# Kernel optimization log

Hardware: AMD Instinct MI355X
Metric: run time of the kernel (lower is better)

The kernel has to match this reference:

```python
import jax, jax.numpy as jnp
import numpy as np

# Assumptions from DCalhas/eeg_to_fmri repo layers:
#  - RandomFourierFeatures: z = cos(x @ W + b) followed by layer normalization
#    over the feature axis (normalization='layer'), W/b trainable.
#  - Sinusoids: elementwise sin(x).

B, D, T, L = 64, 512, 1024, 512

def _layer_norm(x, eps=1e-5):
    mu = jnp.mean(x, axis=-1, keepdims=True)
    var = jnp.var(x, axis=-1, keepdims=True)
    return (x - mu) * jax.lax.rsqrt(var + eps)

def setup_inputs() -> dict:
    key = jax.random.key(0)
    ks = jax.random.split(key, 12)
    s = 1.0 / np.sqrt(L)
    return {
        "x": jax.random.normal(ks[0], (B, D, T), jnp.float32),
        "rff_w": jax.random.normal(ks[1], (D, L), jnp.float32) * (1.0 / np.sqrt(D)),
        "rff_b": jax.random.uniform(ks[2], (L,), jnp.float32, 0.0, 2.0 * np.pi),
        "weight_input": jax.random.normal(ks[3], (L, L), jnp.float32) * s,
        "weight_forget": jax.random.normal(ks[4], (L, L), jnp.float32) * s,
        "weight_context": jax.random.normal(ks[5], (L, L), jnp.float32) * s,
        "recurrent_input": jax.random.normal(ks[6], (L, L), jnp.float32) * s,
        "recurrent_forget": jax.random.normal(ks[7], (L, L), jnp.float32) * s,
        "recurrent_context": jax.random.normal(ks[8], (L, L), jnp.float32) * s,
        "bias_input": jnp.zeros((L,), jnp.float32),
        "bias_forget": jnp.zeros((L,), jnp.float32),
        "bias_context": jnp.zeros((L,), jnp.float32),
        "init_latent": jax.random.normal(ks[9], (1, 1, L), jnp.float32) * s,
        "init_context": jax.random.normal(ks[10], (1, 1, L), jnp.float32) * s,
    }

def reference(x, rff_w, rff_b, weight_input, weight_forget, weight_context,
              recurrent_input, recurrent_forget, recurrent_context,
              bias_input, bias_forget, bias_context, init_latent, init_context):
    b = x.shape[0]
    xt = jnp.transpose(x, (0, 2, 1))                      # [B,T,D]
    z = _layer_norm(jnp.cos(xt @ rff_w + rff_b))          # [B,T,L]
    # hidden_states[t+1] = z_t in the original loop, so the "recurrent" input
    # at step t is z_{t-1} (init_latent at t=0). Gates are thus batchable.
    z_prev = jnp.concatenate(
        [jnp.broadcast_to(init_latent, (b, 1, z.shape[2])), z[:, :-1]], axis=1)
    i = jax.nn.sigmoid(z @ weight_input + z_prev @ recurrent_input + bias_input)
    f = jax.nn.sigmoid(z @ weight_forget + z_prev @ recurrent_forget + bias_forget)
    g = jnp.tanh(z @ weight_context + z_prev @ recurrent_context + bias_context)
    o = jnp.sin(z)                                        # Sinusoids gate

    c0 = jnp.broadcast_to(init_context[:, 0], (b, z.shape[2]))  # [B,L]
    def step(c_prev, gates):
        i_t, f_t, g_t, o_t = gates
        c_t = f_t * c_prev + i_t * g_t
        return c_t, o_t * c_t
    xs = tuple(jnp.transpose(a, (1, 0, 2)) for a in (i, f, g, o))  # time-major
    _, h = jax.lax.scan(step, c0, xs)                     # [T,B,L]
    return jnp.transpose(h, (1, 2, 0))                    # [B,L,T]
```

## Files before the change

### kernel.cpp

```cpp
#include <hip/hip_runtime.h>
#include <hip/hip_bf16.h>
#include <hip/hip_fp16.h>
#include <cstdint>
#include <cstddef>


typedef float f32x4 __attribute__((ext_vector_type(4)));
typedef short s16x8 __attribute__((ext_vector_type(8)));

__device__ __forceinline__ void gload_lds16(const void* g, void* l) {
  __builtin_amdgcn_global_load_lds(
      (const __attribute__((address_space(1))) void*)g,
      (__attribute__((address_space(3))) void*)l, 16, 0, 0);
}
__device__ __forceinline__ ushort f2bf(float f) {
  uint32_t u = __float_as_uint(f);
  return (ushort)((u + 0x7FFF + ((u >> 16) & 1)) >> 16);
}
__device__ __forceinline__ float bf2f(ushort s) {
  return __uint_as_float(((uint32_t)s) << 16);
}
__device__ __forceinline__ ushort f2h(float f) {
  return __half_as_ushort(__float2half(f));
}
__device__ __forceinline__ float h2f(ushort s) {
  return __half2float(__ushort_as_half(s));
}

#define MF(d, a, b) d = __builtin_amdgcn_mfma_f32_16x16x32_bf16(a, b, d, 0, 0, 0);

__global__ __launch_bounds__(256) void prep_all(
    const float* __restrict__ s0, const float* __restrict__ s1,
    const float* __restrict__ s2, const float* __restrict__ s3,
    const float* __restrict__ s4, const float* __restrict__ s5,
    const float* __restrict__ il, const float* __restrict__ W1,
    const float* __restrict__ x,
    ushort* __restrict__ W2t, ushort* __restrict__ ilb,
    ushort* __restrict__ W1t, ushort* __restrict__ xt)
{
  __shared__ float tile[64][68];
  const int z = blockIdx.z;
  if (z >= 8) {
    if (blockIdx.y >= 8) return;
    const int b = z - 8;
    const int t0 = blockIdx.x * 64, d0 = blockIdx.y * 64;
    const float* src = x + ((size_t)b * 512 + d0) * 1024 + t0;
    const int lr_ = threadIdx.x >> 4, lc4 = (threadIdx.x & 15) * 4;
#pragma unroll
    for (int p = 0; p < 4; ++p) {
      const float4 v = *(const float4*)(src + (size_t)(lr_ + p * 16) * 1024 + lc4);
      *(float4*)&tile[lr_ + p * 16][lc4] = v;
    }
    __syncthreads();
    const int tt = threadIdx.x >> 2, dc = (threadIdx.x & 3) * 16;
    ushort* dst = xt + ((size_t)b * 1024 + t0 + tt) * 512 + d0 + dc;
    uint4 o1, o2;
    o1.x = (uint)f2bf(tile[dc + 0][tt]) | ((uint)f2bf(tile[dc + 1][tt]) << 16);
    o1.y = (uint)f2bf(tile[dc + 2][tt]) | ((uint)f2bf(tile[dc + 3][tt]) << 16);
    o1.z = (uint)f2bf(tile[dc + 4][tt]) | ((uint)f2bf(tile[dc + 5][tt]) << 16);
    o1.w = (uint)f2bf(tile[dc + 6][tt]) | ((uint)f2bf(tile[dc + 7][tt]) << 16);
    o2.x = (uint)f2bf(tile[dc + 8][tt]) | ((uint)f2bf(tile[dc + 9][tt]) << 16);
    o2.y = (uint)f2bf(tile[dc + 10][tt]) | ((uint)f2bf(tile[dc + 11][tt]) << 16);
    o2.z = (uint)f2bf(tile[dc + 12][tt]) | ((uint)f2bf(tile[dc + 13][tt]) << 16);
    o2.w = (uint)f2bf(tile[dc + 14][tt]) | ((uint)f2bf(tile[dc + 15][tt]) << 16);
    *(uint4*)(dst) = o1;
    *(uint4*)(dst + 8) = o2;
    return;
  }
  if (z == 6) {
    if (blockIdx.x == 0 && blockIdx.y == 0) {
      ilb[threadIdx.x] = f2bf(il[threadIdx.x]);
      ilb[threadIdx.x + 256] = f2bf(il[threadIdx.x + 256]);
    }
    return;
  }
  const float* src = z == 0 ? s0 : z == 1 ? s1 : z == 2 ? s2
                   : z == 3 ? s3 : z == 4 ? s4 : z == 5 ? s5 : W1;
  ushort* dst = (z == 7) ? W1t
              : W2t + (size_t)(z >> 1) * 512 * 1024 + (z & 1) * 512;
  const int ld = (z == 7) ? 512 : 1024;
  float (*t32)[33] = (float(*)[33])&tile[0][0];
  const int c0 = blockIdx.x * 32, r0 = blockIdx.y * 32;
  const int tx = threadIdx.x & 31, ty = threadIdx.x >> 5;
#pragma unroll
  for (int i = 0; i < 4; ++i)
    t32[ty + i * 8][tx] = src[(size_t)(r0 + ty + i * 8) * 512 + c0 + tx];
  __syncthreads();
#pragma unroll
  for (int i = 0; i < 4; ++i)
    dst[(size_t)(c0 + ty + i * 8) * ld + r0 + tx] = f2bf(t32[tx][ty + i * 8]);
}

__global__ __launch_bounds__(256, 2) void k1_mfma(
    const ushort* __restrict__ A, const ushort* __restrict__ Bt,
    const float* __restrict__ bias, ushort* __restrict__ U)
{
  __shared__ __align__(16) short As[128 * 64];
  __shared__ __align__(16) short Bs[128 * 64];
  const int tid = threadIdx.x;
  const int lane = tid & 63, wid = tid >> 6;
  const int orig = blockIdx.x;
  const int swz = (orig & 7) * 256 + (orig >> 3);
  const int n0 = (swz & 3) * 128, r0 = (swz >> 2) * 128;
  const int wr = wid >> 1, wc = wid & 1;
  const int fr = lane & 15, fq = lane >> 4;
  const int lr = lane >> 3;
  const int swz_el = ((lane & 7) ^ lr) * 8;

  const int RA = r0 + wid * 32 + lr;
  const ushort* pa0 = A + (size_t)(RA)      * 512 + swz_el;
  const ushort* pa1 = A + (size_t)(RA + 8)  * 512 + swz_el;
  const ushort* pa2 = A + (size_t)(RA + 16) * 512 + swz_el;
  const ushort* pa3 = A + (size_t)(RA + 24) * 512 + swz_el;
  const int RB = n0 + wid * 32 + lr;
  const ushort* pb0 = Bt + (size_t)(RB)      * 512 + swz_el;
  const ushort* pb1 = Bt + (size_t)(RB + 8)  * 512 + swz_el;
  const ushort* pb2 = Bt + (size_t)(RB + 16) * 512 + swz_el;
  const ushort* pb3 = Bt + (size_t)(RB + 24) * 512 + swz_el;
  char* dA = (char*)As + wid * 4096;
  char* dB = (char*)Bs + wid * 4096;

  const int so0 = fr * 64 + ((fq)     ^ (fr & 7)) * 8;
  const int so1 = fr * 64 + ((4 + fq) ^ (fr & 7)) * 8;

  f32x4 c00 = {0.f,0.f,0.f,0.f}, c01 = c00, c02 = c00, c03 = c00,
        c10 = c00, c11 = c00, c12 = c00, c13 = c00,
        c20 = c00, c21 = c00, c22 = c00, c23 = c00,
        c30 = c00, c31 = c00, c32 = c00, c33 = c00;

  for (int k0 = 0; k0 < 512; k0 += 64) {
    gload_lds16(pa0 + k0, dA);        gload_lds16(pa1 + k0, dA + 1024);
    gload_lds16(pa2 + k0, dA + 2048); gload_lds16(pa3 + k0, dA + 3072);
    gload_lds16(pb0 + k0, dB);        gload_lds16(pb1 + k0, dB + 1024);
    gload_lds16(pb2 + k0, dB + 2048); gload_lds16(pb3 + k0, dB + 3072);
    __syncthreads();
    const s16x8 a00 = *(const s16x8*)&As[wr * 4096 + 0 * 1024 + so0];
    const s16x8 a01 = *(const s16x8*)&As[wr * 4096 + 0 * 1024 + so1];
    const s16x8 a10 = *(const s16x8*)&As[wr * 4096 + 1 * 1024 + so0];
    const s16x8 a11 = *(const s16x8*)&As[wr * 4096 + 1 * 1024 + so1];
    const s16x8 a20 = *(const s16x8*)&As[wr * 4096 + 2 * 1024 + so0];
    const s16x8 a21 = *(const s16x8*)&As[wr * 4096 + 2 * 1024 + so1];
    const s16x8 a30 = *(const s16x8*)&As[wr * 4096 + 3 * 1024 + so0];
    const s16x8 a31 = *(const s16x8*)&As[wr * 4096 + 3 * 1024 + so1];
    const s16x8 b00 = *(const s16x8*)&Bs[wc * 4096 + 0 * 1024 + so0];
    const s16x8 b01 = *(const s16x8*)&Bs[wc * 4096 + 0 * 1024 + so1];
    const s16x8 b10 = *(const s16x8*)&Bs[wc * 4096 + 1 * 1024 + so0];
    const s16x8 b11 = *(const s16x8*)&Bs[wc * 4096 + 1 * 1024 + so1];
    const s16x8 b20 = *(const s16x8*)&Bs[wc * 4096 + 2 * 1024 + so0];
    const s16x8 b21 = *(const s16x8*)&Bs[wc * 4096 + 2 * 1024 + so1];
    const s16x8 b30 = *(const s16x8*)&Bs[wc * 4096 + 3 * 1024 + so0];
    const s16x8 b31 = *(const s16x8*)&Bs[wc * 4096 + 3 * 1024 + so1];
    MF(c00, a00, b00) MF(c01, a00, b10) MF(c02, a00, b20) MF(c03, a00, b30)
    MF(c10, a10, b00) MF(c11, a10, b10) MF(c12, a10, b20) MF(c13, a10, b30)
    MF(c20, a20, b00) MF(c21, a20, b10) MF(c22, a20, b20) MF(c23, a20, b30)
    MF(c30, a30, b00) MF(c31, a30, b10) MF(c32, a30, b20) MF(c33, a30, b30)
    MF(c00, a01, b01) MF(c01, a01, b11) MF(c02, a01, b21) MF(c03, a01, b31)
    MF(c10, a11, b01) MF(c11, a11, b11) MF(c12, a11, b21) MF(c13, a11, b31)
    MF(c20, a21, b01) MF(c21, a21, b11) MF(c22, a21, b21) MF(c23, a21, b31)
    MF(c30, a31, b01) MF(c31, a31, b11) MF(c32, a31, b21) MF(c33, a31, b31)
    __syncthreads();
  }

#define EPI1(cmn, m_, n_) { \
    const int col = n0 + wc * 64 + n_ * 16 + fr; \
    const float bv = bias[col]; \
    const int rbase = r0 + wr * 64 + m_ * 16 + fq * 4; \
    _Pragma("unroll") for (int j = 0; j < 4; ++j) \
      U[(size_t)(rbase + j) * 512 + col] = f2bf(cosf(cmn[j] + bv)); }
  EPI1(c00, 0, 0) EPI1(c01, 0, 1) EPI1(c02, 0, 2) EPI1(c03, 0, 3)
  EPI1(c10, 1, 0) EPI1(c11, 1, 1) EPI1(c12, 1, 2) EPI1(c13, 1, 3)
  EPI1(c20, 2, 0) EPI1(c21, 2, 1) EPI1(c22, 2, 2) EPI1(c23, 2, 3)
  EPI1(c30, 3, 0) EPI1(c31, 3, 1) EPI1(c32, 3, 2) EPI1(c33, 3, 3)
#undef EPI1
}

__global__ __launch_bounds__(256) void ln_rows(
    const ushort* __restrict__ U, ushort* __restrict__ Z)
{
  const int row = blockIdx.x * 4 + (threadIdx.x >> 6);
  const int lane = threadIdx.x & 63;
  const size_t base = (size_t)row * 512 + lane * 8;
  const uint4 pk = *(const uint4*)(U + base);
  float v[8];
  v[0] = bf2f(pk.x & 0xffff); v[1] = bf2f(pk.x >> 16);
  v[2] = bf2f(pk.y & 0xffff); v[3] = bf2f(pk.y >> 16);
  v[4] = bf2f(pk.z & 0xffff); v[5] = bf2f(pk.z >> 16);
  v[6] = bf2f(pk.w & 0xffff); v[7] = bf2f(pk.w >> 16);
  float s = 0.f, s2 = 0.f;
#pragma unroll
  for (int j = 0; j < 8; ++j) { s += v[j]; s2 += v[j] * v[j]; }
#pragma unroll
  for (int m = 1; m < 64; m <<= 1) { s += __shfl_xor(s, m); s2 += __shfl_xor(s2, m); }
  const float mean = s * (1.f / 512.f);
  const float var = s2 * (1.f / 512.f) - mean * mean;
  const float inv = rsqrtf(var + 1e-5f);
  uint4 o;
  o.x = (uint)f2bf((v[0] - mean) * inv) | ((uint)f2bf((v[1] - mean) * inv) << 16);
  o.y = (uint)f2bf((v[2] - mean) * inv) | ((uint)f2bf((v[3] - mean) * inv) << 16);
  o.z = (uint)f2bf((v[4] - mean) * inv) | ((uint)f2bf((v[5] - mean) * inv) << 16);
  o.w = (uint)f2bf((v[6] - mean) * inv) | ((uint)f2bf((v[7] - mean) * inv) << 16);
  *(uint4*)(Z + base) = o;
}

__global__ __launch_bounds__(256, 2) void k2_mfma(
    const ushort* __restrict__ Z, const ushort* __restrict__ Wt,
    const ushort* __restrict__ IL,
    const float* __restrict__ biv, const float* __restrict__ bfv,
    const float* __restrict__ bcv,
    ushort* __restrict__ G2, int tc, int Tc, int nwg)
{
  __shared__ __align__(16) short As[128 * 64];
  __shared__ __align__(16) short Bs0[128 * 64];
  __shared__ __align__(16) short Bs1[128 * 64];
  const int tid = threadIdx.x;
  const int lane = tid & 63, wid = tid >> 6;
  const int cpx = nwg >> 3;
  const int orig = blockIdx.x;
  const int swz = (orig & 7) * cpx + (orig >> 3);
  const int bx = swz % 6, by = swz / 6;
  const int nb = Tc >> 7;
  const int b = by / nb, tb = by % nb;
  const int r0g = b * 1024 + tc + tb * 128;
  const int r0c = b * Tc + tb * 128;
  const bool isig = bx < 4;
  const int n0 = isig ? bx * 128 : 0;
  const int fb = bx - 4;
  const int wr = wid >> 1, wc = wid & 1;
  const int fr = lane & 15, fq = lane >> 4;
  const int lr = lane >> 3;
  const int swz_el = ((lane & 7) ^ lr) * 8;

  const int R0 = r0g + wid * 32 + lr;
  const ushort* pa0 = Z + (size_t)(R0)      * 512 + swz_el;
  const ushort* pa1 = Z + (size_t)(R0 + 8)  * 512 + swz_el;
  const ushort* pa2 = Z + (size_t)(R0 + 16) * 512 + swz_el;
  const ushort* pa3 = Z + (size_t)(R0 + 24) * 512 + swz_el;
  const ushort* ph0 = ((((R0)      & 1023) == 0) ? IL : (Z + (size_t)(R0 - 1)  * 512)) + swz_el;
  const ushort* ph1 = ((((R0 + 8)  & 1023) == 0) ? IL : (Z + (size_t)(R0 + 7)  * 512)) + swz_el;
  const ushort* ph2 = ((((R0 + 16) & 1023) == 0) ? IL : (Z + (size_t)(R0 + 15) * 512)) + swz_el;
  const ushort* ph3 = ((((R0 + 24) & 1023) == 0) ? IL : (Z + (size_t)(R0 + 23) * 512)) + swz_el;
  const int RB0 = (isig ? n0 : 512 + fb * 256) + wid * 32 + lr;
  const ushort* pb0 = Wt + (size_t)(RB0)      * 1024 + swz_el;
  const ushort* pb1 = Wt + (size_t)(RB0 + 8)  * 1024 + swz_el;
  const ushort* pb2 = Wt + (size_t)(RB0 + 16) * 1024 + swz_el;
  const ushort* pb3 = Wt + (size_t)(RB0 + 24) * 1024 + swz_el;
  const int RB1 = (isig ? 1024 + n0 : 512 + fb * 256 + 128) + wid * 32 + lr;
  const ushort* pq0 = Wt + (size_t)(RB1)      * 1024 + swz_el;
  const ushort* pq1 = Wt + (size_t)(RB1 + 8)  * 1024 + swz_el;
  const ushort* pq2 = Wt + (size_t)(RB1 + 16) * 1024 + swz_el;
  const ushort* pq3 = Wt + (size_t)(RB1 + 24) * 1024 + swz_el;

  const int so0 = fr * 64 + ((fq)     ^ (fr & 7)) * 8;
  const int so1 = fr * 64 + ((4 + fq) ^ (fr & 7)) * 8;

  f32x4 zz = {0.f,0.f,0.f,0.f};
  f32x4 c00=zz,c01=zz,c02=zz,c03=zz, c10=zz,c11=zz,c12=zz,c13=zz,
        c20=zz,c21=zz,c22=zz,c23=zz, c30=zz,c31=zz,c32=zz,c33=zz;
  f32x4 d00=zz,d01=zz,d02=zz,d03=zz, d10=zz,d11=zz,d12=zz,d13=zz,
        d20=zz,d21=zz,d22=zz,d23=zz, d30=zz,d31=zz,d32=zz,d33=zz;

#define STG8(P0,P1,P2,P3, KO, DST) { \
    char* d_ = (char*)(DST) + wid * 4096; \
    gload_lds16((P0) + (KO), d_);        gload_lds16((P1) + (KO), d_ + 1024); \
    gload_lds16((P2) + (KO), d_ + 2048); gload_lds16((P3) + (KO), d_ + 3072); }

#define RDA(SO) \
    const s16x8 fa0 = *(const s16x8*)&As[wr * 4096 + 0 * 1024 + (SO)]; \
    const s16x8 fa1 = *(const s16x8*)&As[wr * 4096 + 1 * 1024 + (SO)]; \
    const s16x8 fa2 = *(const s16x8*)&As[wr * 4096 + 2 * 1024 + (SO)]; \
    const s16x8 fa3 = *(const s16x8*)&As[wr * 4096 + 3 * 1024 + (SO)];

#define RDB(BS, SO) \
    const s16x8 fb0 = *(const s16x8*)&(BS)[wc * 4096 + 0 * 1024 + (SO)]; \
    const s16x8 fb1 = *(const s16x8*)&(BS)[wc * 4096 + 1 * 1024 + (SO)]; \
    const s16x8 fb2 = *(const s16x8*)&(BS)[wc * 4096 + 2 * 1024 + (SO)]; \
    const s16x8 fb3 = *(const s16x8*)&(BS)[wc * 4096 + 3 * 1024 + (SO)];

#define MMC \
    MF(c00,fa0,fb0) MF(c01,fa0,fb1) MF(c02,fa0,fb2) MF(c03,fa0,fb3) \
    MF(c10,fa1,fb0) MF(c11,fa1,fb1) MF(c12,fa1,fb2) MF(c13,fa1,fb3) \
    MF(c20,fa2,fb0) MF(c21,fa2,fb1) MF(c22,fa2,fb2) MF(c23,fa2,fb3) \
    MF(c30,fa3,fb0) MF(c31,fa3,fb1) MF(c32,fa3,fb2) MF(c33,fa3,fb3)

#define MMD \
    MF(d00,fa0,fb0) MF(d01,fa0,fb1) MF(d02,fa0,fb2) MF(d03,fa0,fb3) \
    MF(d10,fa1,fb0) MF(d11,fa1,fb1) MF(d12,fa1,fb2) MF(d13,fa1,fb3) \
    MF(d20,fa2,fb0) MF(d21,fa2,fb1) MF(d22,fa2,fb2) MF(d23,fa2,fb3) \
    MF(d30,fa3,fb0) MF(d31,fa3,fb1) MF(d32,fa3,fb2) MF(d33,fa3,fb3)

#define KSTEP(SO_) { \
    RDA(SO_) \
    { RDB(Bs0, SO_) MMC } \
    { RDB(Bs1, SO_) MMD } }

  for (int k0 = 0; k0 < 512; k0 += 64) {
    STG8(pa0, pa1, pa2, pa3, k0, As)
    STG8(pb0, pb1, pb2, pb3, k0, Bs0)
    STG8(pq0, pq1, pq2, pq3, k0, Bs1)
    __syncthreads();
    KSTEP(so0)
    KSTEP(so1)
    __syncthreads();
  }
  for (int k0 = 0; k0 < 512; k0 += 64) {
    STG8(ph0, ph1, ph2, ph3, k0, As)
    STG8(pb0, pb1, pb2, pb3, 512 + k0, Bs0)
    STG8(pq0, pq1, pq2, pq3, 512 + k0, Bs1)
    __syncthreads();
    KSTEP(so0)
    KSTEP(so1)
    __syncthreads();
  }
#undef KSTEP
#undef MMD
#undef MMC
#undef RDB
#undef RDA
#undef STG8

  if (isig) {
#define EPI(cmn, dmn, m_, n_) { \
    const int col = n0 + wc * 64 + n_ * 16 + fr; \
    const float bvi = biv[col], bvc = bcv[col]; \
    const int rbase = wr * 64 + m_ * 16 + fq * 4; \
    _Pragma("unroll") for (int j = 0; j < 4; ++j) { \
      const float iv = 1.f / (1.f + __expf(-(cmn[j] + bvi))); \
      const float gv = 2.f / (1.f + __expf(-2.f * (dmn[j] + bvc))) - 1.f; \
      G2[(size_t)(r0c + rbase + j) * 1024 + col] = f2h(iv * gv); } }
    EPI(c00, d00, 0, 0) EPI(c01, d01, 0, 1) EPI(c02, d02, 0, 2) EPI(c03, d03, 0, 3)
    EPI(c10, d10, 1, 0) EPI(c11, d11, 1, 1) EPI(c12, d12, 1, 2) EPI(c13, d13, 1, 3)
    EPI(c20, d20, 2, 0) EPI(c21, d21, 2, 1) EPI(c22, d22, 2, 2) EPI(c23, d23, 2, 3)
    EPI(c30, d30, 3, 0) EPI(c31, d31, 3, 1) EPI(c32, d32, 3, 2) EPI(c33, d33, 3, 3)
#undef EPI
  } else {
#define EPIF(cmn, m_, n_, COFF) { \
    const int col = fb * 256 + (COFF) + wc * 64 + n_ * 16 + fr; \
    const float bv = bfv[col]; \
    const int rbase = wr * 64 + m_ * 16 + fq * 4; \
    _Pragma("unroll") for (int j = 0; j < 4; ++j) { \
      const float fv = 1.f / (1.f + __expf(-(cmn[j] + bv))); \
      G2[(size_t)(r0c + rbase + j) * 1024 + 512 + col] = f2h(fv); } }
    EPIF(c00, 0, 0, 0) EPIF(c01, 0, 1, 0) EPIF(c02, 0, 2, 0) EPIF(c03, 0, 3, 0)
    EPIF(c10, 1, 0, 0) EPIF(c11, 1, 1, 0) EPIF(c12, 1, 2, 0) EPIF(c13, 1, 3, 0)
    EPIF(c20, 2, 0, 0) EPIF(c21, 2, 1, 0) EPIF(c22, 2, 2, 0) EPIF(c23, 2, 3, 0)
    EPIF(c30, 3, 0, 0) EPIF(c31, 3, 1, 0) EPIF(c32, 3, 2, 0) EPIF(c33, 3, 3, 0)
    EPIF(d00, 0, 0, 128) EPIF(d01, 0, 1, 128) EPIF(d02, 0, 2, 128) EPIF(d03, 0, 3, 128)
    EPIF(d10, 1, 0, 128) EPIF(d11, 1, 1, 128) EPIF(d12, 1, 2, 128) EPIF(d13, 1, 3, 128)
    EPIF(d20, 2, 0, 128) EPIF(d21, 2, 1, 128) EPIF(d22, 2, 2, 128) EPIF(d23, 2, 3, 128)
    EPIF(d30, 3, 0, 128) EPIF(d31, 3, 1, 128) EPIF(d32, 3, 2, 128) EPIF(d33, 3, 3, 128)
#undef EPIF
  }
}

__global__ __launch_bounds__(256) void k3a_seg(
    const ushort* __restrict__ G2, float* __restrict__ Aseg,
    float* __restrict__ Bseg, int Tc)
{
  const int l2 = threadIdx.x * 2;
  const int b = blockIdx.x, s = blockIdx.y;
  const int SEGc = Tc >> 6;
  const ushort* gb = G2 + ((size_t)(b * Tc + s * 64)) * 1024;
  float A0 = 1.f, A1 = 1.f, c0 = 0.f, c1 = 0.f;
#pragma unroll 8
  for (int j = 0; j < 64; ++j) {
    const uint Pp = *(const uint*)(gb + (size_t)j * 1024 + l2);
    const uint Fp = *(const uint*)(gb + (size_t)j * 1024 + 512 + l2);
    const float P0 = h2f((ushort)(Pp & 0xffff)), P1 = h2f((ushort)(Pp >> 16));
    const float F0 = h2f((ushort)(Fp & 0xffff)), F1 = h2f((ushort)(Fp >> 16));
    A0 *= F0; A1 *= F1;
    c0 = fmaf(F0, c0, P0); c1 = fmaf(F1, c1, P1);
  }
  const size_t o = (size_t)(b * SEGc + s) * 512 + l2;
  float2 av; av.x = A0; av.y = A1;
  float2 bv; bv.x = c0; bv.y = c1;
  *(float2*)(Aseg + o) = av;
  *(float2*)(Bseg + o) = bv;
}

__global__ __launch_bounds__(128) void k3c_emit(
    const ushort* __restrict__ G2, const ushort* __restrict__ Z,
    const float* __restrict__ Aseg, const float* __restrict__ Bseg,
    const float* __restrict__ initc, float* __restrict__ cbuf,
    float* __restrict__ out, int tc, int Tc)
{
  __shared__ float tile[128][65];
  const int tid = threadIdx.x;
  const int l0 = blockIdx.x * 128;
  const int b = blockIdx.y, s = blockIdx.z;
  const int SEGc = Tc >> 6;
  const int l = l0 + tid;

  float c = (tc == 0) ? initc[l] : cbuf[b * 512 + l];
#pragma unroll
  for (int sp = 0; sp < 15; ++sp) {
    const size_t o = (size_t)(b * SEGc + sp) * 512 + l;
    const float Av = Aseg[o], Bv = Bseg[o];
    c = (sp < s) ? fmaf(Av, c, Bv) : c;
  }

  const ushort* gb = G2 + ((size_t)(b * Tc + s * 64)) * 1024 + l;
  const ushort* zb = Z + ((size_t)(b * 1024 + tc + s * 64)) * 512 + l;
#pragma unroll 8
  for (int j = 0; j < 64; ++j) {
    const float P = h2f(gb[(size_t)j * 1024]);
    const float F = h2f(gb[(size_t)j * 1024 + 512]);
    const float zv = bf2f(zb[(size_t)j * 512]);
    c = fmaf(F, c, P);
    tile[tid][j] = sinf(zv) * c;
  }
  if (s == SEGc - 1) cbuf[b * 512 + l] = c;
  __syncthreads();
  const int col = tid & 63, rhalf = tid >> 6;
  const size_t obase = ((size_t)b * 512 + l0) * 1024 + (size_t)(tc + s * 64) + col;
#pragma unroll
  for (int p = 0; p < 64; ++p) {
    const int row = rhalf + p * 2;
    out[obase + (size_t)row * 1024] = tile[row][col];
  }
}

extern "C" void kernel_launch(void* const* d_in, const int* in_sizes, int n_in,
                              void* d_out, int out_size, void* d_ws, size_t ws_size,
                              hipStream_t stream)
{
  const float* x  = (const float*)d_in[0];
  const float* W  = (const float*)d_in[1];
  const float* rb = (const float*)d_in[2];
  const float* wi = (const float*)d_in[3];
  const float* wf = (const float*)d_in[4];
  const float* wc = (const float*)d_in[5];
  const float* ri = (const float*)d_in[6];
  const float* rf = (const float*)d_in[7];
  const float* rc = (const float*)d_in[8];
  const float* bi = (const float*)d_in[9];
  const float* bfo = (const float*)d_in[10];
  const float* bc = (const float*)d_in[11];
  const float* il = (const float*)d_in[12];
  const float* ic = (const float*)d_in[13];
  float* out = (float*)d_out;

  char* ws = (char*)d_ws;
  size_t off = 0;
  auto alloc = [&](size_t bytes) -> void* {
    void* p = ws + off;
    off = (off + bytes + 255) & ~(size_t)255;
    return p;
  };
  ushort* z    = (ushort*)alloc((size_t)65536 * 512 * 2);
  ushort* W1t  = (ushort*)alloc((size_t)512 * 512 * 2);
  ushort* W2t  = (ushort*)alloc((size_t)1536 * 1024 * 2);
  ushort* ilb  = (ushort*)alloc(512 * 2);
  float*  cbuf = (float*)alloc((size_t)64 * 512 * 4);
  float*  Aseg = (float*)alloc((size_t)64 * 16 * 512 * 4);
  float*  Bseg = (float*)alloc((size_t)64 * 16 * 512 * 4);
  const size_t fixed_end = off;
  ushort* xt   = (ushort*)alloc((size_t)65536 * 512 * 2);
  ushort* G2   = (ushort*)(ws + fixed_end);
  ushort* u    = (ushort*)d_out;

  int Tc = 1024;
  while (Tc > 128 && fixed_end + (size_t)64 * Tc * 1024 * 2 > ws_size) Tc >>= 1;

  prep_all<<<dim3(16, 16, 72), 256, 0, stream>>>(
      wi, ri, wf, rf, wc, rc, il, W, x, W2t, ilb, W1t, xt);

  k1_mfma<<<dim3(2048), 256, 0, stream>>>(xt, W1t, rb, u);
  ln_rows<<<16384, 256, 0, stream>>>(u, z);

  for (int tc = 0; tc < 1024; tc += Tc) {
    const int SEGc = Tc >> 6;
    const int nwg2 = 6 * 64 * (Tc >> 7);
    k2_mfma<<<dim3(nwg2), 256, 0, stream>>>(
        z, W2t, ilb, bi, bfo, bc, G2, tc, Tc, nwg2);
    k3a_seg<<<dim3(64, SEGc), 256, 0, stream>>>(G2, Aseg, Bseg, Tc);
    k3c_emit<<<dim3(4, 64, SEGc), 128, 0, stream>>>(
        G2, z, Aseg, Bseg, ic, cbuf, out, tc, Tc);
  }
}
```

Baseline: 532.9 us.

## Fuse x transpose and bf16 conversion into the first GEMM's A-tile load

The separate transpose of x into a bf16 [B,T,D] buffer is removed. The first GEMM now reads fp32 x directly, converts it to bf16 and writes the swizzled A tile into LDS itself. This saves a full 128 MB read plus 64 MB write/read round trip. In exchange, each k-step in the GEMM does synchronous scalar strided global loads and LDS stores instead of async direct-to-LDS loads, and x is re-read once for each of the 4 N-tiles.

```diff
diff --git a/kernel.cpp b/kernel.cpp
--- a/kernel.cpp
+++ b/kernel.cpp
@@ -34,39 +34,11 @@
     const float* __restrict__ s2, const float* __restrict__ s3,
     const float* __restrict__ s4, const float* __restrict__ s5,
     const float* __restrict__ il, const float* __restrict__ W1,
-    const float* __restrict__ x,
     ushort* __restrict__ W2t, ushort* __restrict__ ilb,
-    ushort* __restrict__ W1t, ushort* __restrict__ xt)
-{
-  __shared__ float tile[64][68];
+    ushort* __restrict__ W1t)
+{
+  __shared__ float tile[32][33];
   const int z = blockIdx.z;
-  if (z >= 8) {
-    if (blockIdx.y >= 8) return;
-    const int b = z - 8;
-    const int t0 = blockIdx.x * 64, d0 = blockIdx.y * 64;
-    const float* src = x + ((size_t)b * 512 + d0) * 1024 + t0;
-    const int lr_ = threadIdx.x >> 4, lc4 = (threadIdx.x & 15) * 4;
-#pragma unroll
-    for (int p = 0; p < 4; ++p) {
-      const float4 v = *(const float4*)(src + (size_t)(lr_ + p * 16) * 1024 + lc4);
-      *(float4*)&tile[lr_ + p * 16][lc4] = v;
-    }
-    __syncthreads();
-    const int tt = threadIdx.x >> 2, dc = (threadIdx.x & 3) * 16;
-    ushort* dst = xt + ((size_t)b * 1024 + t0 + tt) * 512 + d0 + dc;
-    uint4 o1, o2;
-    o1.x = (uint)f2bf(tile[dc + 0][tt]) | ((uint)f2bf(tile[dc + 1][tt]) << 16);
-    o1.y = (uint)f2bf(tile[dc + 2][tt]) | ((uint)f2bf(tile[dc + 3][tt]) << 16);
-    o1.z = (uint)f2bf(tile[dc + 4][tt]) | ((uint)f2bf(tile[dc + 5][tt]) << 16);
-    o1.w = (uint)f2bf(tile[dc + 6][tt]) | ((uint)f2bf(tile[dc + 7][tt]) << 16);
-    o2.x = (uint)f2bf(tile[dc + 8][tt]) | ((uint)f2bf(tile[dc + 9][tt]) << 16);
-    o2.y = (uint)f2bf(tile[dc + 10][tt]) | ((uint)f2bf(tile[dc + 11][tt]) << 16);
-    o2.z = (uint)f2bf(tile[dc + 12][tt]) | ((uint)f2bf(tile[dc + 13][tt]) << 16);
-    o2.w = (uint)f2bf(tile[dc + 14][tt]) | ((uint)f2bf(tile[dc + 15][tt]) << 16);
-    *(uint4*)(dst) = o1;
-    *(uint4*)(dst + 8) = o2;
-    return;
-  }
   if (z == 6) {
     if (blockIdx.x == 0 && blockIdx.y == 0) {
       ilb[threadIdx.x] = f2bf(il[threadIdx.x]);
@@ -79,20 +51,19 @@
   ushort* dst = (z == 7) ? W1t
               : W2t + (size_t)(z >> 1) * 512 * 1024 + (z & 1) * 512;
   const int ld = (z == 7) ? 512 : 1024;
-  float (*t32)[33] = (float(*)[33])&tile[0][0];
   const int c0 = blockIdx.x * 32, r0 = blockIdx.y * 32;
   const int tx = threadIdx.x & 31, ty = threadIdx.x >> 5;
 #pragma unroll
   for (int i = 0; i < 4; ++i)
-    t32[ty + i * 8][tx] = src[(size_t)(r0 + ty + i * 8) * 512 + c0 + tx];
+    tile[ty + i * 8][tx] = src[(size_t)(r0 + ty + i * 8) * 512 + c0 + tx];
   __syncthreads();
 #pragma unroll
   for (int i = 0; i < 4; ++i)
-    dst[(size_t)(c0 + ty + i * 8) * ld + r0 + tx] = f2bf(t32[tx][ty + i * 8]);
+    dst[(size_t)(c0 + ty + i * 8) * ld + r0 + tx] = f2bf(tile[tx][ty + i * 8]);
 }
 
 __global__ __launch_bounds__(256, 2) void k1_mfma(
-    const ushort* __restrict__ A, const ushort* __restrict__ Bt,
+    const float* __restrict__ x, const ushort* __restrict__ Bt,
     const float* __restrict__ bias, ushort* __restrict__ U)
 {
   __shared__ __align__(16) short As[128 * 64];
@@ -102,22 +73,20 @@
   const int orig = blockIdx.x;
   const int swz = (orig & 7) * 256 + (orig >> 3);
   const int n0 = (swz & 3) * 128, r0 = (swz >> 2) * 128;
+  const int b = r0 >> 10, t0 = r0 & 1023;
   const int wr = wid >> 1, wc = wid & 1;
   const int fr = lane & 15, fq = lane >> 4;
   const int lr = lane >> 3;
   const int swz_el = ((lane & 7) ^ lr) * 8;
 
-  const int RA = r0 + wid * 32 + lr;
-  const ushort* pa0 = A + (size_t)(RA)      * 512 + swz_el;
-  const ushort* pa1 = A + (size_t)(RA + 8)  * 512 + swz_el;
-  const ushort* pa2 = A + (size_t)(RA + 16) * 512 + swz_el;
-  const ushort* pa3 = A + (size_t)(RA + 24) * 512 + swz_el;
+  const float* xb = x + ((size_t)b * 512) * 1024 + t0;
+  const int tA = tid & 127, hA = tid >> 7;
+
   const int RB = n0 + wid * 32 + lr;
   const ushort* pb0 = Bt + (size_t)(RB)      * 512 + swz_el;
   const ushort* pb1 = Bt + (size_t)(RB + 8)  * 512 + swz_el;
   const ushort* pb2 = Bt + (size_t)(RB + 16) * 512 + swz_el;
   const ushort* pb3 = Bt + (size_t)(RB + 24) * 512 + swz_el;
-  char* dA = (char*)As + wid * 4096;
   char* dB = (char*)Bs + wid * 4096;
 
   const int so0 = fr * 64 + ((fq)     ^ (fr & 7)) * 8;
@@ -129,10 +98,23 @@
         c30 = c00, c31 = c00, c32 = c00, c33 = c00;
 
   for (int k0 = 0; k0 < 512; k0 += 64) {
-    gload_lds16(pa0 + k0, dA);        gload_lds16(pa1 + k0, dA + 1024);
-    gload_lds16(pa2 + k0, dA + 2048); gload_lds16(pa3 + k0, dA + 3072);
     gload_lds16(pb0 + k0, dB);        gload_lds16(pb1 + k0, dB + 1024);
     gload_lds16(pb2 + k0, dB + 2048); gload_lds16(pb3 + k0, dB + 3072);
+#pragma unroll
+    for (int q = 0; q < 4; ++q) {
+      const int c = hA * 4 + q;
+      const float* src = xb + (size_t)(k0 + c * 8) * 1024 + tA;
+      const float v0 = src[0 * 1024], v1 = src[1 * 1024];
+      const float v2 = src[2 * 1024], v3 = src[3 * 1024];
+      const float v4 = src[4 * 1024], v5 = src[5 * 1024];
+      const float v6 = src[6 * 1024], v7 = src[7 * 1024];
+      uint4 o;
+      o.x = (uint)f2bf(v0) | ((uint)f2bf(v1) << 16);
+      o.y = (uint)f2bf(v2) | ((uint)f2bf(v3) << 16);
+      o.z = (uint)f2bf(v4) | ((uint)f2bf(v5) << 16);
+      o.w = (uint)f2bf(v6) | ((uint)f2bf(v7) << 16);
+      *(uint4*)&As[tA * 64 + ((c ^ (tA & 7)) * 8)] = o;
+    }
     __syncthreads();
     const s16x8 a00 = *(const s16x8*)&As[wr * 4096 + 0 * 1024 + so0];
     const s16x8 a01 = *(const s16x8*)&As[wr * 4096 + 0 * 1024 + so1];
@@ -454,17 +436,16 @@
   float*  Aseg = (float*)alloc((size_t)64 * 16 * 512 * 4);
   float*  Bseg = (float*)alloc((size_t)64 * 16 * 512 * 4);
   const size_t fixed_end = off;
-  ushort* xt   = (ushort*)alloc((size_t)65536 * 512 * 2);
   ushort* G2   = (ushort*)(ws + fixed_end);
   ushort* u    = (ushort*)d_out;
 
   int Tc = 1024;
   while (Tc > 128 && fixed_end + (size_t)64 * Tc * 1024 * 2 > ws_size) Tc >>= 1;
 
-  prep_all<<<dim3(16, 16, 72), 256, 0, stream>>>(
-      wi, ri, wf, rf, wc, rc, il, W, x, W2t, ilb, W1t, xt);
-
-  k1_mfma<<<dim3(2048), 256, 0, stream>>>(xt, W1t, rb, u);
+  prep_all<<<dim3(16, 16, 8), 256, 0, stream>>>(
+      wi, ri, wf, rf, wc, rc, il, W, W2t, ilb, W1t);
+
+  k1_mfma<<<dim3(2048), 256, 0, stream>>>(x, W1t, rb, u);
   ln_rows<<<16384, 256, 0, stream>>>(u, z);
 
   for (int tc = 0; tc < 1024; tc += Tc) {
```

Measured after the change: 510.0 us. 4.3% less time.
